# Kernel tuning notes

Measured on AMD Instinct MI355X. Metric: run time of the kernel, lower is better.

## Reference

```python
import jax, jax.numpy as jnp
import numpy as np
import math

# Model hyperparameters (match init_kwargs)
B, S, E = 8, 1024, 512
NUM_HEADS = 8
NQ = 16        # n_qubits for quantum attention
NQF = 16       # n_qubits_ffn for quantum feed-forward
FFN = 2048
L = 4          # num_layers
EPS = 1e-5


def _sinusoidal_pe(seq_len, embed_dim):
    pos = np.arange(seq_len)[:, None].astype(np.float32)
    div = np.exp(np.arange(0, embed_dim, 2).astype(np.float32) * (-math.log(10000.0) / embed_dim))
    pe = np.zeros((seq_len, embed_dim), dtype=np.float32)
    pe[:, 0::2] = np.sin(pos * div)
    pe[:, 1::2] = np.cos(pos * div)
    return jnp.asarray(pe)


def setup_inputs() -> dict:
    key = jax.random.key(0)
    ks = jax.random.split(key, 12)
    x = jax.random.normal(ks[0], (B, S, E), dtype=jnp.float32)
    pe = _sinusoidal_pe(S, E)
    # per-layer parameters stacked along leading L axis
    theta_attn = jax.random.normal(ks[1], (L, NQ), dtype=jnp.float32) * 0.1   # RY angles (attention circuit)
    theta_ffn = jax.random.normal(ks[2], (L, NQF), dtype=jnp.float32) * 0.1    # RY angles (ffn circuit)
    W_combine = jax.random.normal(ks[3], (L, E, NQ), dtype=jnp.float32) / math.sqrt(NQ)
    W1 = jax.random.normal(ks[4], (L, FFN, NQF), dtype=jnp.float32) / math.sqrt(NQF)
    W2 = jax.random.normal(ks[5], (L, E, FFN), dtype=jnp.float32) / math.sqrt(FFN)
    g1 = jnp.ones((L, E), dtype=jnp.float32)
    b1 = jnp.zeros((L, E), dtype=jnp.float32)
    g2 = jnp.ones((L, E), dtype=jnp.float32)
    b2 = jnp.zeros((L, E), dtype=jnp.float32)
    return {"x": x, "pe": pe, "theta_attn": theta_attn, "theta_ffn": theta_ffn,
            "W_combine": W_combine, "W1": W1, "W2": W2,
            "g1": g1, "b1": b1, "g2": g2, "b2": b2}


def _layer_norm(h, g, b):
    m = jnp.mean(h, axis=-1, keepdims=True)
    v = jnp.var(h, axis=-1, keepdims=True)
    return (h - m) * jax.lax.rsqrt(v + EPS) * g + b


def _quantum_features(h, theta, n_qubits):
    # Each wire: |0> -> RX(x_i) -> RY(theta_i) -> <Z_i> = cos(theta_i) * cos(x_i)
    # Product state => exact closed form; vectorizes the per-token circuit loop.
    return jnp.cos(theta)[None, None, :] * jnp.cos(h[..., :n_qubits])


def reference(x, pe, theta_attn, theta_ffn, W_combine, W1, W2, g1, b1, g2, b2):
    b_, s_, e_ = x.shape
    dk = NQ // NUM_HEADS
    h = x + pe[None, :s_, :]
    for l in range(L):
        qv = _quantum_features(h, theta_attn[l], NQ)                 # [B,S,NQ]
        q = qv.reshape(b_, s_, NUM_HEADS, dk).transpose(0, 2, 1, 3)  # [B,H,S,dk]
        scores = jnp.einsum('bhqd,bhkd->bhqk', q, q) / math.sqrt(dk)
        probs = jax.nn.softmax(scores, axis=-1)
        attn = jnp.einsum('bhqk,bhkd->bhqd', probs, q)               # [B,H,S,dk]
        attn = attn.transpose(0, 2, 1, 3).reshape(b_, s_, NQ)
        attn_out = attn @ W_combine[l].T                             # [B,S,E]
        h = _layer_norm(h + attn_out, g1[l], b1[l])
        # --- quantum feed-forward ---
        qf = _quantum_features(h, theta_ffn[l], NQF)                 # [B,S,NQF]
        ffn_out = jax.nn.relu(qf @ W1[l].T) @ W2[l].T                # [B,S,E]
        h = _layer_norm(h + ffn_out, g2[l], b2[l])
    return h
```

## Files before the change

### kernel.cpp

```cpp
#include <hip/hip_runtime.h>
#include <cstdint>
#include <cstddef>

#define BB 8
#define SS 1024
#define EE 512
#define NQB 16
#define FF 2048

typedef unsigned short u16;
typedef __attribute__((ext_vector_type(8))) short short8;
typedef __attribute__((ext_vector_type(4))) float f32x4;
typedef unsigned int uint_g __attribute__((address_space(1)));
typedef unsigned int uint_l __attribute__((address_space(3)));

#define FLAG_OFF   0
#define ATTN_OFF   4096
#define QF_OFF     528384
#define W1P_OFF    1052672
#define STATS_OFF  1314816
#define H_OFF      2097152
#define W2P_OFF    18874368

__device__ __forceinline__ float u2f(u16 u){ return __uint_as_float(((unsigned)u)<<16); }
__device__ __forceinline__ u16 f2bf(float x){
  unsigned u = __float_as_uint(x);
  u += 0x7FFF + ((u>>16)&1);
  return (u16)(u>>16);
}
__device__ __forceinline__ float ldg(const void* p,int f,size_t i){
  return f ? ((const float*)p)[i] : u2f(((const u16*)p)[i]);
}
__device__ __forceinline__ float4 ldg4(const void* p,int f,size_t i){
  float4 r;
  if (f){ r = ((const float4*)p)[i>>2]; }
  else { ushort4 v = ((const ushort4*)p)[i>>2];
         r.x=u2f(v.x); r.y=u2f(v.y); r.z=u2f(v.z); r.w=u2f(v.w); }
  return r;
}
__device__ __forceinline__ short8 ldfrag8(const void* p,int f,size_t i){
  short8 r;
  if (f){
    float4 A  = ((const float4*)p)[i>>2];
    float4 Bv = ((const float4*)p)[(i>>2)+1];
    r[0]=(short)f2bf(A.x);  r[1]=(short)f2bf(A.y);  r[2]=(short)f2bf(A.z);  r[3]=(short)f2bf(A.w);
    r[4]=(short)f2bf(Bv.x); r[5]=(short)f2bf(Bv.y); r[6]=(short)f2bf(Bv.z); r[7]=(short)f2bf(Bv.w);
  } else {
    r = *(const short8*)((const u16*)p + i);
  }
  return r;
}
__device__ __forceinline__ void async16(const void* g, void* l){
  __builtin_amdgcn_global_load_lds((const uint_g*)g, (uint_l*)l, 16, 0, 0);
}
__device__ __forceinline__ void tok_stats(const float* st, int tok, float& m, float& rs){
  float S1 = 0.f, S2 = 0.f;
  #pragma unroll
  for (int nb=0; nb<4; ++nb){
    float2 p = *(const float2*)&st[((size_t)tok*4+nb)*2];
    S1 += p.x; S2 += p.y;
  }
  m = S1*(1.f/512.f);
  float var = S2*(1.f/512.f) - m*m;
  rs = rsqrtf(var + 1e-5f);
}

__global__ void detect_k(const u16* __restrict__ x, int* __restrict__ flag){
  __shared__ int cnt;
  if (threadIdx.x==0) cnt=0;
  __syncthreads();
  int c=0;
  for (int i=threadIdx.x;i<4096;i+=256){
    u16 v = x[(size_t)i*2];
    int ex = (v>>7)&0xFF;
    c += (ex>=160) ? 1 : 0;
  }
  atomicAdd(&cnt,c);
  __syncthreads();
  if (threadIdx.x==0) *flag = (cnt>64) ? 1 : 0;
}

__global__ __launch_bounds__(256) void w1pack_k(const void* __restrict__ W1,
    const void* __restrict__ thf, u16* __restrict__ W1p, const int* __restrict__ flag){
  int f = *flag;
  int idx = blockIdx.x*256 + threadIdx.x;
  int l = idx>>12, nt = (idx>>5)&127, lane32 = idx&31;
  int quad = lane32>>4, col = lane32&15;
  short8 v = ldfrag8(W1, f, ((size_t)l*FF + nt*16 + col)*16 + quad*8);
  short8 o;
  #pragma unroll
  for (int j=0;j<8;++j){
    float th = ldg(thf, f, (size_t)l*16 + quad*8 + j);
    o[j] = (short)f2bf(__cosf(th) * u2f((u16)v[j]));
  }
  *(short8*)(W1p + (size_t)idx*8) = o;
}

__global__ __launch_bounds__(256) void w2pack_k(const void* __restrict__ W2,
    u16* __restrict__ W2p, const int* __restrict__ flag){
  int f = *flag;
  int idx = blockIdx.x*256 + threadIdx.x;
  int lane = idx&63, kb = (idx>>6)&63, teg = (idx>>12)&31, l = idx>>17;
  int quad = lane>>4, col = lane&15;
  short8 v = ldfrag8(W2, f, ((size_t)l*EE + teg*16 + col)*FF + kb*32 + quad*8);
  *(short8*)(W2p + (size_t)idx*8) = v;
}

__global__ __launch_bounds__(256) void add_pe_k(const void* __restrict__ x,
    const void* __restrict__ pe, float* __restrict__ hw, const int* __restrict__ flag){
  int f = *flag;
  size_t e = ((size_t)blockIdx.x*256 + threadIdx.x)*4;
  float4 xv = ldg4(x,f,e);
  float4 pv = ldg4(pe,f,e & (size_t)(SS*EE-1));
  float4 o; o.x=xv.x+pv.x; o.y=xv.y+pv.y; o.z=xv.z+pv.z; o.w=xv.w+pv.w;
  *(float4*)&hw[e] = o;
}

__global__ __launch_bounds__(1024) void attn3_k(const float* __restrict__ hw,
    const void* __restrict__ theta, float* __restrict__ attn,
    const float* __restrict__ st, const void* __restrict__ g2,
    const void* __restrict__ b2, const int* __restrict__ flag, int lazy, int l){
  __shared__ float q0[SS], q1[SS];
  __shared__ float part[SS*3];
  int f = *flag;
  int b = blockIdx.x>>3, hd = blockIdx.x&7;
  int tid = threadIdx.x;
  float c0 = __cosf(ldg(theta,f,(size_t)l*16 + hd*2));
  float c1 = __cosf(ldg(theta,f,(size_t)l*16 + hd*2+1));
  float ga0=1.f, gb0=0.f, ga1=1.f, gb1=0.f;
  if (lazy){
    size_t gb = (size_t)(l-1)*EE + hd*2;
    ga0 = ldg(g2,f,gb);   gb0 = ldg(b2,f,(size_t)(l-1)*EE + hd*2);
    ga1 = ldg(g2,f,gb+1); gb1 = ldg(b2,f,(size_t)(l-1)*EE + hd*2+1);
  }
  size_t hb = (size_t)b*SS*EE + hd*2;
  {
    int j = tid;
    float v0 = hw[hb + (size_t)j*EE];
    float v1 = hw[hb + (size_t)j*EE + 1];
    if (lazy){
      float m, rs; tok_stats(st, b*SS + j, m, rs);
      v0 = fmaf((v0-m)*rs, ga0, gb0);
      v1 = fmaf((v1-m)*rs, ga1, gb1);
    }
    q0[j] = c0*__cosf(v0);
    q1[j] = c1*__cosf(v1);
  }
  __syncthreads();
  int rloc = tid & 255, kz = tid >> 8;
  int r = blockIdx.y*256 + rloc;
  const float sc = 0.70710678118f;
  float a0 = q0[r]*sc, a1 = q1[r]*sc;
  float den=0.f, n0=0.f, n1=0.f;
  int j0 = kz*256;
  for (int j=j0; j<j0+256; ++j){
    float u0=q0[j], u1=q1[j];
    float e = __expf(fmaf(a1,u1, a0*u0));
    den += e; n0 = fmaf(e,u0,n0); n1 = fmaf(e,u1,n1);
  }
  part[(rloc*4+kz)*3+0]=den; part[(rloc*4+kz)*3+1]=n0; part[(rloc*4+kz)*3+2]=n1;
  __syncthreads();
  if (tid < 256){
    int rr = blockIdx.y*256 + tid;
    float d=0.f, s0=0.f, s1=0.f;
    #pragma unroll
    for (int k=0;k<4;++k){
      d  += part[(tid*4+k)*3+0];
      s0 += part[(tid*4+k)*3+1];
      s1 += part[(tid*4+k)*3+2];
    }
    float inv = 1.f/d;
    float* ap = attn + ((size_t)(b*SS + rr))*NQB + hd*2;
    ap[0]=s0*inv; ap[1]=s1*inv;
  }
}

__global__ __launch_bounds__(256) void combine2_k(float* __restrict__ hw,
    const float* __restrict__ attn, const void* __restrict__ Wc,
    const void* __restrict__ g1v, const void* __restrict__ b1v,
    const void* __restrict__ g2v, const void* __restrict__ b2v,
    const float* __restrict__ st, float* __restrict__ qf,
    const int* __restrict__ flag, int lazy, int l){
  __shared__ float AFR[32*16];
  __shared__ float MS[32], RS[32];
  __shared__ float outC[32*520];
  int f = *flag;
  int tid = threadIdx.x, tok0 = blockIdx.x*32;
  for (int u=tid; u<512; u+=256)
    AFR[u] = attn[(size_t)(tok0 + (u>>4))*16 + (u&15)];
  if (lazy && tid<32){
    float m, rs; tok_stats(st, tok0+tid, m, rs);
    MS[tid]=m; RS[tid]=rs;
  }
  __syncthreads();
  int e0 = tid*2;
  float wc0[16], wc1[16];
  size_t wb = (size_t)l*EE*16;
  #pragma unroll
  for (int q4=0;q4<4;++q4){
    float4 a = ldg4(Wc,f, wb + (size_t)e0*16     + q4*4);
    float4 b = ldg4(Wc,f, wb + (size_t)(e0+1)*16 + q4*4);
    wc0[q4*4+0]=a.x; wc0[q4*4+1]=a.y; wc0[q4*4+2]=a.z; wc0[q4*4+3]=a.w;
    wc1[q4*4+0]=b.x; wc1[q4*4+1]=b.y; wc1[q4*4+2]=b.z; wc1[q4*4+3]=b.w;
  }
  float gl0=1.f,bl0=0.f,gl1=1.f,bl1=0.f;
  if (lazy){
    size_t gb = (size_t)(l-1)*EE;
    gl0 = ldg(g2v,f,gb+e0);   bl0 = ldg(b2v,f,gb+e0);
    gl1 = ldg(g2v,f,gb+e0+1); bl1 = ldg(b2v,f,gb+e0+1);
  }
  for (int t=0; t<32; ++t){
    float2 hr = *(const float2*)&hw[(size_t)(tok0+t)*EE + e0];
    float v0 = hr.x, v1 = hr.y;
    if (lazy){
      float m = MS[t], rs = RS[t];
      v0 = fmaf((v0-m)*rs, gl0, bl0);
      v1 = fmaf((v1-m)*rs, gl1, bl1);
    }
    float s0 = v0, s1 = v1;
    #pragma unroll
    for (int q4=0;q4<4;++q4){
      float4 av = *(const float4*)&AFR[t*16 + q4*4];
      s0 = fmaf(av.x, wc0[q4*4+0], fmaf(av.y, wc0[q4*4+1], fmaf(av.z, wc0[q4*4+2], fmaf(av.w, wc0[q4*4+3], s0))));
      s1 = fmaf(av.x, wc1[q4*4+0], fmaf(av.y, wc1[q4*4+1], fmaf(av.z, wc1[q4*4+2], fmaf(av.w, wc1[q4*4+3], s1))));
    }
    outC[t*520 + e0] = s0; outC[t*520 + e0 + 1] = s1;
  }
  __syncthreads();
  {
    int token = tid>>3, prt = tid&7;
    float s=0.f, s2=0.f;
    #pragma unroll 8
    for (int i2=0;i2<64;++i2){
      float vv = outC[token*520 + prt + 8*i2];
      s += vv; s2 = fmaf(vv,vv,s2);
    }
    #pragma unroll
    for (int off=4; off; off>>=1){ s += __shfl_down(s,off,8); s2 += __shfl_down(s2,off,8); }
    if (prt==0){
      float m = s*(1.f/512.f);
      float var = s2*(1.f/512.f) - m*m;
      MS[token] = m; RS[token] = rsqrtf(var+1e-5f);
    }
  }
  __syncthreads();
  for (int u=tid; u<32*128; u+=256){
    int tok = u>>7, c4 = (u&127)*4;
    float4 vv = *(const float4*)&outC[tok*520 + c4];
    float m = MS[tok], rs = RS[tok];
    float4 gv = ldg4(g1v,f,(size_t)l*EE + c4);
    float4 bv = ldg4(b1v,f,(size_t)l*EE + c4);
    float4 o;
    o.x = fmaf((vv.x-m)*rs, gv.x, bv.x);
    o.y = fmaf((vv.y-m)*rs, gv.y, bv.y);
    o.z = fmaf((vv.z-m)*rs, gv.z, bv.z);
    o.w = fmaf((vv.w-m)*rs, gv.w, bv.w);
    *(float4*)&hw[(size_t)(tok0+tok)*EE + c4] = o;
    if (c4 < 16){
      float4 qo;
      qo.x=__cosf(o.x); qo.y=__cosf(o.y); qo.z=__cosf(o.z); qo.w=__cosf(o.w);
      *(float4*)&qf[(size_t)(tok0+tok)*16 + c4] = qo;
    }
  }
}

__global__ __launch_bounds__(256) void ffn3_k(float* __restrict__ hw,
    const float* __restrict__ qf, const u16* __restrict__ W1p,
    const void* __restrict__ W2, const u16* __restrict__ W2p,
    float* __restrict__ st, const int* __restrict__ flag, int cv, int l){
  __shared__ float SMF[8704];
  u16* HtA = (u16*)SMF;
  u16* W2t = (u16*)SMF + 4096;
  float* outL = SMF;

  int f = *flag;
  int tid = threadIdx.x, w = tid>>6, lane = tid&63;
  int quad = lane>>4, col = lane&15;
  int mb = blockIdx.x, nb = blockIdx.y;
  int tok0 = mb*64;
  int wm = w&1, wn = w>>1;

  short8 a0[4];
  #pragma unroll
  for (int mt=0; mt<4; ++mt){
    short8 z = {0,0,0,0,0,0,0,0};
    if (quad < 2){
      const float* qp = qf + (size_t)(tok0 + mt*16 + col)*16 + quad*8;
      float4 A = *(const float4*)qp, B = *(const float4*)(qp+4);
      z[0]=(short)f2bf(A.x); z[1]=(short)f2bf(A.y); z[2]=(short)f2bf(A.z); z[3]=(short)f2bf(A.w);
      z[4]=(short)f2bf(B.x); z[5]=(short)f2bf(B.y); z[6]=(short)f2bf(B.z); z[7]=(short)f2bf(B.w);
    }
    a0[mt] = z;
  }

  f32x4 acc[2][4];
  #pragma unroll
  for (int i=0;i<2;++i)
    #pragma unroll
    for (int j=0;j<4;++j) acc[i][j] = (f32x4){0.f,0.f,0.f,0.f};
  const f32x4 zc = {0.f,0.f,0.f,0.f};
  size_t w2base = (size_t)l*EE*FF;

  for (int k0=0; k0<FF; k0+=64){
    if (cv){
      #pragma unroll
      for (int fi=0; fi<4; ++fi){
        int slot = w*4+fi, te = slot>>1, s = slot&1;
        int kb = (k0>>5) + s;
        const u16* gp = W2p + (((size_t)l*32 + nb*8 + te)*64 + kb)*512 + lane*8;
        async16(gp, &W2t[slot*512]);
      }
    } else {
      #pragma unroll
      for (int fi=0; fi<4; ++fi){
        int slot = w*4+fi, te = slot>>1, s = slot&1;
        short8 v = ldfrag8(W2, f, w2base + (size_t)(nb*128 + te*16 + col)*FF + k0 + s*32 + quad*8);
        *(short8*)&W2t[slot*512 + lane*8] = v;
      }
    }
    short8 b1 = {0,0,0,0,0,0,0,0};
    if (quad < 2)
      b1 = *(const short8*)(W1p + (((size_t)l*128 + (k0>>4) + w)*32 + quad*16 + col)*8);
    int s1w = w>>1, koff = (w&1)*16;
    int lane2 = ((koff + col)>>3)*16 + quad*4;
    int jj = col&7;
    #pragma unroll
    for (int mt=0; mt<4; ++mt){
      f32x4 hc = __builtin_amdgcn_mfma_f32_16x16x32_bf16(a0[mt], b1, zc, 0,0,0);
      #pragma unroll
      for (int r=0;r<4;++r)
        HtA[(mt*2+s1w)*512 + (lane2+r)*8 + jj] = f2bf(fmaxf(hc[r], 0.f));
    }
    __syncthreads();
    #pragma unroll
    for (int s=0;s<2;++s){
      short8 A2[2], B2[4];
      A2[0] = *(const short8*)&HtA[((wm*2+0)*2+s)*512 + lane*8];
      A2[1] = *(const short8*)&HtA[((wm*2+1)*2+s)*512 + lane*8];
      #pragma unroll
      for (int et=0;et<4;++et)
        B2[et] = *(const short8*)&W2t[((wn*4+et)*2+s)*512 + lane*8];
      #pragma unroll
      for (int et=0;et<4;++et){
        acc[0][et] = __builtin_amdgcn_mfma_f32_16x16x32_bf16(A2[0], B2[et], acc[0][et], 0,0,0);
        acc[1][et] = __builtin_amdgcn_mfma_f32_16x16x32_bf16(A2[1], B2[et], acc[1][et], 0,0,0);
      }
    }
    __syncthreads();
  }

  #pragma unroll
  for (int mt2=0; mt2<2; ++mt2){
    #pragma unroll
    for (int r=0;r<4;++r){
      int ltok = wm*32 + mt2*16 + quad*4 + r;
      size_t hb = (size_t)(tok0+ltok)*EE + nb*128;
      #pragma unroll
      for (int et=0;et<4;++et){
        int eloc = wn*64 + et*16 + col;
        outL[ltok*132 + eloc] = acc[mt2][et][r] + hw[hb + eloc];
      }
    }
  }
  __syncthreads();
  {
    int token = tid>>2, prt = tid&3;
    float s=0.f, s2=0.f;
    #pragma unroll 8
    for (int i2=0;i2<32;++i2){
      float vv = outL[token*132 + prt + 4*i2];
      s += vv; s2 = fmaf(vv,vv,s2);
    }
    s += __shfl_down(s,2,4); s2 += __shfl_down(s2,2,4);
    s += __shfl_down(s,1,4); s2 += __shfl_down(s2,1,4);
    if (prt==0){
      float2 o; o.x = s; o.y = s2;
      *(float2*)&st[((size_t)(tok0+token)*4 + nb)*2] = o;
    }
  }
  for (int u=tid; u<64*32; u+=256){
    int tok = u>>5, c4 = (u&31)*4;
    float4 vv = *(const float4*)&outL[tok*132 + c4];
    *(float4*)&hw[(size_t)(tok0+tok)*EE + nb*128 + c4] = vv;
  }
}

__global__ __launch_bounds__(256) void conv2_k(const float* __restrict__ hw,
    const float* __restrict__ st, const void* __restrict__ g2v,
    const void* __restrict__ b2v, void* __restrict__ out,
    const int* __restrict__ flag){
  int f = *flag;
  size_t i = (size_t)blockIdx.x*256 + threadIdx.x;
  int tok = (int)(i>>7), c4 = ((int)i&127)*4;
  float4 v = *(const float4*)&hw[i*4];
  float m, rs; tok_stats(st, tok, m, rs);
  float4 gv = ldg4(g2v,f,(size_t)3*EE + c4);
  float4 bv = ldg4(b2v,f,(size_t)3*EE + c4);
  float4 o;
  o.x = fmaf((v.x-m)*rs, gv.x, bv.x);
  o.y = fmaf((v.y-m)*rs, gv.y, bv.y);
  o.z = fmaf((v.z-m)*rs, gv.z, bv.z);
  o.w = fmaf((v.w-m)*rs, gv.w, bv.w);
  if (f){
    *(float4*)((float*)out + i*4) = o;
  } else {
    ushort4 ob; ob.x=f2bf(o.x); ob.y=f2bf(o.y); ob.z=f2bf(o.z); ob.w=f2bf(o.w);
    *(ushort4*)((u16*)out + i*4) = ob;
  }
}

extern "C" void kernel_launch(void* const* d_in, const int* in_sizes, int n_in,
                              void* d_out, int out_size, void* d_ws, size_t ws_size,
                              hipStream_t stream) {
  (void)in_sizes; (void)n_in; (void)out_size;
  char* ws = (char*)d_ws;
  int*   flag = (int*)(ws + FLAG_OFF);
  float* attn = (float*)(ws + ATTN_OFF);
  float* qf   = (float*)(ws + QF_OFF);
  u16*   w1p  = (u16*)(ws + W1P_OFF);
  float* st   = (float*)(ws + STATS_OFF);
  float* hw   = (float*)(ws + H_OFF);
  u16*   w2p  = (u16*)(ws + W2P_OFF);
  int cv = (ws_size >= (size_t)W2P_OFF + ((size_t)8<<20)) ? 1 : 0;

  detect_k<<<1,256,0,stream>>>((const u16*)d_in[0], flag);
  w1pack_k<<<64,256,0,stream>>>(d_in[5], d_in[3], w1p, flag);
  if (cv) w2pack_k<<<2048,256,0,stream>>>(d_in[6], w2p, flag);
  add_pe_k<<<4096,256,0,stream>>>(d_in[0], d_in[1], hw, flag);
  for (int l=0; l<4; ++l){
    int lazy = (l>0) ? 1 : 0;
    attn3_k<<<dim3(64,4),1024,0,stream>>>(hw, d_in[2], attn, st,
                                          d_in[9], d_in[10], flag, lazy, l);
    combine2_k<<<256,256,0,stream>>>(hw, attn, d_in[4], d_in[7], d_in[8],
                                     d_in[9], d_in[10], st, qf, flag, lazy, l);
    ffn3_k<<<dim3(128,4),256,0,stream>>>(hw, qf, w1p, d_in[6], w2p,
                                         st, flag, cv, l);
  }
  conv2_k<<<4096,256,0,stream>>>(hw, st, d_in[9], d_in[10], d_out, flag);
}
```

Measured before the change: 443.6 us.

## Fuse attention into combine kernel, double-buffer FFN stages, separate first-16 residual buffer

Merges the attention kernel into the combine kernel, so each 256-thread block recomputes the quantum features for all 1024 tokens of its batch in shared memory and computes attention for its 32 tokens across all 8 heads. This removes one launch and the global attention buffer round trip. The FFN kernel now double-buffers its W2 staging and its hidden-activation tiles, which drops one barrier per k-step and lets the next stage load overlap the current MFMAs. The first 16 columns of h are written to a separate h16 buffer so combine does not overwrite hw columns that other blocks in the same kernel still read. The cost is that every block redoes the feature computation for the whole batch, and attention now runs on 256 blocks of 256 threads each looping over 1024 keys instead of a 4-way key split, which reduces parallelism.

After: 448.3 us. About the same (+1.1%).

```diff
diff --git a/kernel.cpp b/kernel.cpp
--- a/kernel.cpp
+++ b/kernel.cpp
@@ -15,7 +15,7 @@
 typedef unsigned int uint_l __attribute__((address_space(3)));
 
 #define FLAG_OFF   0
-#define ATTN_OFF   4096
+#define H16_OFF    4096
 #define QF_OFF     528384
 #define W1P_OFF    1052672
 #define STATS_OFF  1314816
@@ -116,81 +116,75 @@
   *(float4*)&hw[e] = o;
 }
 
-__global__ __launch_bounds__(1024) void attn3_k(const float* __restrict__ hw,
-    const void* __restrict__ theta, float* __restrict__ attn,
-    const float* __restrict__ st, const void* __restrict__ g2,
-    const void* __restrict__ b2, const int* __restrict__ flag, int lazy, int l){
-  __shared__ float q0[SS], q1[SS];
-  __shared__ float part[SS*3];
-  int f = *flag;
-  int b = blockIdx.x>>3, hd = blockIdx.x&7;
-  int tid = threadIdx.x;
-  float c0 = __cosf(ldg(theta,f,(size_t)l*16 + hd*2));
-  float c1 = __cosf(ldg(theta,f,(size_t)l*16 + hd*2+1));
-  float ga0=1.f, gb0=0.f, ga1=1.f, gb1=0.f;
-  if (lazy){
-    size_t gb = (size_t)(l-1)*EE + hd*2;
-    ga0 = ldg(g2,f,gb);   gb0 = ldg(b2,f,(size_t)(l-1)*EE + hd*2);
-    ga1 = ldg(g2,f,gb+1); gb1 = ldg(b2,f,(size_t)(l-1)*EE + hd*2+1);
-  }
-  size_t hb = (size_t)b*SS*EE + hd*2;
-  {
-    int j = tid;
-    float v0 = hw[hb + (size_t)j*EE];
-    float v1 = hw[hb + (size_t)j*EE + 1];
-    if (lazy){
-      float m, rs; tok_stats(st, b*SS + j, m, rs);
-      v0 = fmaf((v0-m)*rs, ga0, gb0);
-      v1 = fmaf((v1-m)*rs, ga1, gb1);
-    }
-    q0[j] = c0*__cosf(v0);
-    q1[j] = c1*__cosf(v1);
-  }
-  __syncthreads();
-  int rloc = tid & 255, kz = tid >> 8;
-  int r = blockIdx.y*256 + rloc;
-  const float sc = 0.70710678118f;
-  float a0 = q0[r]*sc, a1 = q1[r]*sc;
-  float den=0.f, n0=0.f, n1=0.f;
-  int j0 = kz*256;
-  for (int j=j0; j<j0+256; ++j){
-    float u0=q0[j], u1=q1[j];
-    float e = __expf(fmaf(a1,u1, a0*u0));
-    den += e; n0 = fmaf(e,u0,n0); n1 = fmaf(e,u1,n1);
-  }
-  part[(rloc*4+kz)*3+0]=den; part[(rloc*4+kz)*3+1]=n0; part[(rloc*4+kz)*3+2]=n1;
-  __syncthreads();
-  if (tid < 256){
-    int rr = blockIdx.y*256 + tid;
-    float d=0.f, s0=0.f, s1=0.f;
-    #pragma unroll
-    for (int k=0;k<4;++k){
-      d  += part[(tid*4+k)*3+0];
-      s0 += part[(tid*4+k)*3+1];
-      s1 += part[(tid*4+k)*3+2];
-    }
-    float inv = 1.f/d;
-    float* ap = attn + ((size_t)(b*SS + rr))*NQB + hd*2;
-    ap[0]=s0*inv; ap[1]=s1*inv;
-  }
-}
-
-__global__ __launch_bounds__(256) void combine2_k(float* __restrict__ hw,
-    const float* __restrict__ attn, const void* __restrict__ Wc,
+__global__ __launch_bounds__(256) void attn_comb_k(float* __restrict__ hw,
+    const void* __restrict__ thA, const void* __restrict__ Wc,
     const void* __restrict__ g1v, const void* __restrict__ b1v,
     const void* __restrict__ g2v, const void* __restrict__ b2v,
-    const float* __restrict__ st, float* __restrict__ qf,
-    const int* __restrict__ flag, int lazy, int l){
-  __shared__ float AFR[32*16];
-  __shared__ float MS[32], RS[32];
-  __shared__ float outC[32*520];
-  int f = *flag;
-  int tid = threadIdx.x, tok0 = blockIdx.x*32;
-  for (int u=tid; u<512; u+=256)
-    AFR[u] = attn[(size_t)(tok0 + (u>>4))*16 + (u&15)];
-  if (lazy && tid<32){
-    float m, rs; tok_stats(st, tok0+tid, m, rs);
-    MS[tid]=m; RS[tid]=rs;
+    const float* __restrict__ st, float* __restrict__ h16,
+    float* __restrict__ qf, const int* __restrict__ flag, int lazy, int l){
+  __shared__ float SM2[19264];
+  float* qq   = SM2;
+  float* outC = SM2;
+  float* msK  = SM2 + 16640;
+  float* AFR  = SM2 + 18688;
+  float* MS   = SM2 + 19200;
+  float* RS   = SM2 + 19232;
+  int f = *flag;
+  int tid = threadIdx.x;
+  int b = blockIdx.x>>5, grp = blockIdx.x&31;
+  size_t bbase = (size_t)b*SS*EE;
+  int tok0 = b*SS + grp*32;
+
+  if (lazy){
+    #pragma unroll
+    for (int t2=0;t2<4;++t2){
+      int j = tid*4+t2;
+      float m, rs; tok_stats(st, b*SS+j, m, rs);
+      msK[j*2]=m; msK[j*2+1]=rs;
+    }
+  }
+  __syncthreads();
+  {
+    int j0 = tid>>2, d0 = (tid&3)*4;
+    float ct[4], gl2[4]={1,1,1,1}, bl2[4]={0,0,0,0};
+    #pragma unroll
+    for (int d=0;d<4;++d) ct[d] = __cosf(ldg(thA,f,(size_t)l*16+d0+d));
+    if (lazy){
+      float4 gv = ldg4(g2v,f,(size_t)(l-1)*EE+d0);
+      float4 bv = ldg4(b2v,f,(size_t)(l-1)*EE+d0);
+      gl2[0]=gv.x; gl2[1]=gv.y; gl2[2]=gv.z; gl2[3]=gv.w;
+      bl2[0]=bv.x; bl2[1]=bv.y; bl2[2]=bv.z; bl2[3]=bv.w;
+    }
+    for (int it=0; it<16; ++it){
+      int j = j0 + it*64;
+      float4 hv = *(const float4*)&hw[bbase + (size_t)j*EE + d0];
+      float vv[4] = {hv.x, hv.y, hv.z, hv.w};
+      if (lazy){
+        float m = msK[j*2], rs = msK[j*2+1];
+        #pragma unroll
+        for (int d=0;d<4;++d) vv[d] = fmaf((vv[d]-m)*rs, gl2[d], bl2[d]);
+      }
+      float4 o;
+      o.x = ct[0]*__cosf(vv[0]); o.y = ct[1]*__cosf(vv[1]);
+      o.z = ct[2]*__cosf(vv[2]); o.w = ct[3]*__cosf(vv[3]);
+      *(float4*)&qq[j*16+d0] = o;
+    }
+  }
+  __syncthreads();
+  {
+    int r = tid&31, hd = tid>>5;
+    int rg = grp*32 + r;
+    float a0 = qq[rg*16 + 2*hd], a1 = qq[rg*16 + 2*hd + 1];
+    const float sc = 0.70710678118f;
+    float a0s = a0*sc, a1s = a1*sc;
+    float den=0.f, n0=0.f, n1=0.f;
+    for (int j=0;j<SS;++j){
+      float2 uv = *(const float2*)&qq[j*16 + 2*hd];
+      float e = __expf(fmaf(a1s, uv.y, a0s*uv.x));
+      den += e; n0 = fmaf(e, uv.x, n0); n1 = fmaf(e, uv.y, n1);
+    }
+    float inv = 1.f/den;
+    AFR[r*16 + 2*hd] = n0*inv; AFR[r*16 + 2*hd + 1] = n1*inv;
   }
   __syncthreads();
   int e0 = tid*2;
@@ -199,9 +193,9 @@
   #pragma unroll
   for (int q4=0;q4<4;++q4){
     float4 a = ldg4(Wc,f, wb + (size_t)e0*16     + q4*4);
-    float4 b = ldg4(Wc,f, wb + (size_t)(e0+1)*16 + q4*4);
+    float4 bq = ldg4(Wc,f, wb + (size_t)(e0+1)*16 + q4*4);
     wc0[q4*4+0]=a.x; wc0[q4*4+1]=a.y; wc0[q4*4+2]=a.z; wc0[q4*4+3]=a.w;
-    wc1[q4*4+0]=b.x; wc1[q4*4+1]=b.y; wc1[q4*4+2]=b.z; wc1[q4*4+3]=b.w;
+    wc1[q4*4+0]=bq.x; wc1[q4*4+1]=bq.y; wc1[q4*4+2]=bq.z; wc1[q4*4+3]=bq.w;
   }
   float gl0=1.f,bl0=0.f,gl1=1.f,bl1=0.f;
   if (lazy){
@@ -213,7 +207,7 @@
     float2 hr = *(const float2*)&hw[(size_t)(tok0+t)*EE + e0];
     float v0 = hr.x, v1 = hr.y;
     if (lazy){
-      float m = MS[t], rs = RS[t];
+      float m = msK[(grp*32+t)*2], rs = msK[(grp*32+t)*2+1];
       v0 = fmaf((v0-m)*rs, gl0, bl0);
       v1 = fmaf((v1-m)*rs, gl1, bl1);
     }
@@ -255,8 +249,10 @@
     o.y = fmaf((vv.y-m)*rs, gv.y, bv.y);
     o.z = fmaf((vv.z-m)*rs, gv.z, bv.z);
     o.w = fmaf((vv.w-m)*rs, gv.w, bv.w);
-    *(float4*)&hw[(size_t)(tok0+tok)*EE + c4] = o;
-    if (c4 < 16){
+    if (c4 >= 16){
+      *(float4*)&hw[(size_t)(tok0+tok)*EE + c4] = o;
+    } else {
+      *(float4*)&h16[(size_t)(tok0+tok)*16 + c4] = o;
       float4 qo;
       qo.x=__cosf(o.x); qo.y=__cosf(o.y); qo.z=__cosf(o.z); qo.w=__cosf(o.w);
       *(float4*)&qf[(size_t)(tok0+tok)*16 + c4] = qo;
@@ -264,13 +260,14 @@
   }
 }
 
-__global__ __launch_bounds__(256) void ffn3_k(float* __restrict__ hw,
-    const float* __restrict__ qf, const u16* __restrict__ W1p,
-    const void* __restrict__ W2, const u16* __restrict__ W2p,
-    float* __restrict__ st, const int* __restrict__ flag, int cv, int l){
-  __shared__ float SMF[8704];
-  u16* HtA = (u16*)SMF;
-  u16* W2t = (u16*)SMF + 4096;
+__global__ __launch_bounds__(256) void ffn4_k(float* __restrict__ hw,
+    const float* __restrict__ h16, const float* __restrict__ qf,
+    const u16* __restrict__ W1p, const void* __restrict__ W2,
+    const u16* __restrict__ W2p, float* __restrict__ st,
+    const int* __restrict__ flag, int cv, int l){
+  __shared__ float SMF[12288];
+  u16* W2t = (u16*)SMF;
+  u16* HtA = (u16*)SMF + 16384;
   float* outL = SMF;
 
   int f = *flag;
@@ -301,53 +298,63 @@
   const f32x4 zc = {0.f,0.f,0.f,0.f};
   size_t w2base = (size_t)l*EE*FF;
 
-  for (int k0=0; k0<FF; k0+=64){
+  auto stage = [&](int k0, int buf){
     if (cv){
       #pragma unroll
       for (int fi=0; fi<4; ++fi){
         int slot = w*4+fi, te = slot>>1, s = slot&1;
         int kb = (k0>>5) + s;
         const u16* gp = W2p + (((size_t)l*32 + nb*8 + te)*64 + kb)*512 + lane*8;
-        async16(gp, &W2t[slot*512]);
+        async16(gp, &W2t[buf*8192 + slot*512 + lane*8]);
       }
     } else {
       #pragma unroll
       for (int fi=0; fi<4; ++fi){
         int slot = w*4+fi, te = slot>>1, s = slot&1;
         short8 v = ldfrag8(W2, f, w2base + (size_t)(nb*128 + te*16 + col)*FF + k0 + s*32 + quad*8);
-        *(short8*)&W2t[slot*512 + lane*8] = v;
+        *(short8*)&W2t[buf*8192 + slot*512 + lane*8] = v;
       }
     }
+  };
+  auto gemm1 = [&](int k0, int buf){
     short8 b1 = {0,0,0,0,0,0,0,0};
     if (quad < 2)
       b1 = *(const short8*)(W1p + (((size_t)l*128 + (k0>>4) + w)*32 + quad*16 + col)*8);
-    int s1w = w>>1, koff = (w&1)*16;
-    int lane2 = ((koff + col)>>3)*16 + quad*4;
-    int jj = col&7;
+    int kl = w*16 + quad*4;
+    int s  = kl>>5, q2 = (kl&31)>>3, j0 = kl&7;
+    u16* dst0 = &HtA[buf*4096 + s*512 + (q2*16+col)*8 + j0];
     #pragma unroll
     for (int mt=0; mt<4; ++mt){
-      f32x4 hc = __builtin_amdgcn_mfma_f32_16x16x32_bf16(a0[mt], b1, zc, 0,0,0);
-      #pragma unroll
-      for (int r=0;r<4;++r)
-        HtA[(mt*2+s1w)*512 + (lane2+r)*8 + jj] = f2bf(fmaxf(hc[r], 0.f));
-    }
+      f32x4 hc = __builtin_amdgcn_mfma_f32_16x16x32_bf16(b1, a0[mt], zc, 0,0,0);
+      ushort4 pk;
+      pk.x = f2bf(fmaxf(hc[0],0.f)); pk.y = f2bf(fmaxf(hc[1],0.f));
+      pk.z = f2bf(fmaxf(hc[2],0.f)); pk.w = f2bf(fmaxf(hc[3],0.f));
+      *(ushort4*)(dst0 + mt*1024) = pk;
+    }
+  };
+
+  stage(0, 0); gemm1(0, 0);
+  for (int i=0; i<32; ++i){
     __syncthreads();
+    int k1 = (i+1)*64;
+    if (k1 < FF){ stage(k1, (i+1)&1); gemm1(k1, (i+1)&1); }
+    int cb = i&1;
     #pragma unroll
     for (int s=0;s<2;++s){
       short8 A2[2], B2[4];
-      A2[0] = *(const short8*)&HtA[((wm*2+0)*2+s)*512 + lane*8];
-      A2[1] = *(const short8*)&HtA[((wm*2+1)*2+s)*512 + lane*8];
+      A2[0] = *(const short8*)&HtA[cb*4096 + ((wm*2+0)*2+s)*512 + lane*8];
+      A2[1] = *(const short8*)&HtA[cb*4096 + ((wm*2+1)*2+s)*512 + lane*8];
       #pragma unroll
       for (int et=0;et<4;++et)
-        B2[et] = *(const short8*)&W2t[((wn*4+et)*2+s)*512 + lane*8];
+        B2[et] = *(const short8*)&W2t[cb*8192 + ((wn*4+et)*2+s)*512 + lane*8];
       #pragma unroll
       for (int et=0;et<4;++et){
         acc[0][et] = __builtin_amdgcn_mfma_f32_16x16x32_bf16(A2[0], B2[et], acc[0][et], 0,0,0);
         acc[1][et] = __builtin_amdgcn_mfma_f32_16x16x32_bf16(A2[1], B2[et], acc[1][et], 0,0,0);
       }
     }
-    __syncthreads();
-  }
+  }
+  __syncthreads();
 
   #pragma unroll
   for (int mt2=0; mt2<2; ++mt2){
@@ -358,7 +365,9 @@
       #pragma unroll
       for (int et=0;et<4;++et){
         int eloc = wn*64 + et*16 + col;
-        outL[ltok*132 + eloc] = acc[mt2][et][r] + hw[hb + eloc];
+        int eg = nb*128 + eloc;
+        float rsd = (eg < 16) ? h16[(size_t)(tok0+ltok)*16 + eg] : hw[hb + eloc];
+        outL[ltok*132 + eloc] = acc[mt2][et][r] + rsd;
       }
     }
   }
@@ -415,7 +424,7 @@
   (void)in_sizes; (void)n_in; (void)out_size;
   char* ws = (char*)d_ws;
   int*   flag = (int*)(ws + FLAG_OFF);
-  float* attn = (float*)(ws + ATTN_OFF);
+  float* h16  = (float*)(ws + H16_OFF);
   float* qf   = (float*)(ws + QF_OFF);
   u16*   w1p  = (u16*)(ws + W1P_OFF);
   float* st   = (float*)(ws + STATS_OFF);
@@ -429,11 +438,10 @@
   add_pe_k<<<4096,256,0,stream>>>(d_in[0], d_in[1], hw, flag);
   for (int l=0; l<4; ++l){
     int lazy = (l>0) ? 1 : 0;
-    attn3_k<<<dim3(64,4),1024,0,stream>>>(hw, d_in[2], attn, st,
-                                          d_in[9], d_in[10], flag, lazy, l);
-    combine2_k<<<256,256,0,stream>>>(hw, attn, d_in[4], d_in[7], d_in[8],
-                                     d_in[9], d_in[10], st, qf, flag, lazy, l);
-    ffn3_k<<<dim3(128,4),256,0,stream>>>(hw, qf, w1p, d_in[6], w2p,
+    attn_comb_k<<<256,256,0,stream>>>(hw, d_in[2], d_in[4], d_in[7], d_in[8],
+                                      d_in[9], d_in[10], st, h16, qf,
+                                      flag, lazy, l);
+    ffn4_k<<<dim3(128,4),256,0,stream>>>(hw, h16, qf, w1p, d_in[6], w2p,
                                          st, flag, cv, l);
   }
   conv2_k<<<4096,256,0,stream>>>(hw, st, d_in[9], d_in[10], d_out, flag);
```
